# Kernel optimization log

Measured on AMD Instinct MI355X. Metric: run time of the kernel, lower is better.

Reference implementation:

```python
import jax, jax.numpy as jnp
import numpy as np

DIM = 1024
HEADS = 16
HEAD_DIM = DIM // HEADS  # 64
WIN = 256
B, N = 4, 4096


def setup_inputs() -> dict:
    key = jax.random.key(0)
    k1, k2, k3 = jax.random.split(key, 3)
    x = jax.random.normal(k1, (B, N, DIM), dtype=jnp.float32)
    # torch nn.Linear weights: [out_features, in_features]
    Wqkv = jax.random.normal(k2, (3 * DIM, DIM), dtype=jnp.float32) * (DIM ** -0.5)
    Wproj = jax.random.normal(k3, (DIM, DIM), dtype=jnp.float32) * (DIM ** -0.5)
    return {"x": x, "Wqkv": Wqkv, "Wproj": Wproj}


def reference(x, Wqkv, Wproj):
    Bs, Ns, C = x.shape
    H, hd, W = HEADS, HEAD_DIM, WIN
    # qkv projection -> [3, B, H, N, hd]
    qkv = (x @ Wqkv.T).reshape(Bs, Ns, 3, H, hd).transpose(2, 0, 3, 1, 4)
    q, k, v = qkv[0], qkv[1], qkv[2]
    q = q * (hd ** -0.5)
    pad = (W - Ns % W) % W
    if pad:
        pw = ((0, 0), (0, 0), (0, pad), (0, 0))
        q = jnp.pad(q, pw)
        k = jnp.pad(k, pw)
        v = jnp.pad(v, pw)
    Np = Ns + pad
    Df = (Np * hd) // W  # flattened feature dim per window row
    q = q.reshape(Bs * H, W, Df)
    k = k.reshape(Bs * H, W, Df)
    v = v.reshape(Bs * H, W, Df)
    attn = jax.nn.softmax(jnp.einsum('bwd,bxd->bwx', q, k), axis=-1)  # [B*H, W, W]
    out = jnp.einsum('bwx,bxd->bwd', attn, v)
    out = out.reshape(Bs, H, Np, hd)[:, :, :Ns, :].transpose(0, 2, 1, 3).reshape(Bs, Ns, C)
    return out @ Wproj.T
```

## Files before the change

### kernel.cpp

```cpp
#include <hip/hip_runtime.h>
#include <hip/hip_bf16.h>
#include <stdint.h>


using u16 = unsigned short;
typedef __attribute__((ext_vector_type(4))) float f32x4;
typedef __attribute__((ext_vector_type(8))) short s16x8;

#define MFMA_BF16(a, b, c) __builtin_amdgcn_mfma_f32_16x16x32_bf16((a), (b), (c), 0, 0, 0)

__device__ __forceinline__ u16 f2bf(float f) {
  union { float f; uint32_t u; } v; v.f = f;
  uint32_t r = v.u + 0x7fffu + ((v.u >> 16) & 1u);
  return (u16)(r >> 16);
}

__device__ __forceinline__ void gld16(const void* g, void* l) {
  auto gp = (const __attribute__((address_space(1))) void*)(uintptr_t)g;
  auto lp = (__attribute__((address_space(3))) void*)(uint32_t)(uintptr_t)l;
  __builtin_amdgcn_global_load_lds(gp, lp, 16, 0, 0);
}

__global__ __launch_bounds__(256) void cvt3(const float* __restrict__ x,
                                            const float* __restrict__ w1,
                                            const float* __restrict__ w2,
                                            u16* __restrict__ ox,
                                            u16* __restrict__ ow1,
                                            u16* __restrict__ ow2) {
  const int stride = gridDim.x * blockDim.x;
  for (int i = blockIdx.x * blockDim.x + threadIdx.x; i < 2621440; i += stride) {
    const float* src; u16* dst; int j;
    if (i < 2097152)      { src = x;  dst = ox;  j = i; }
    else if (i < 2490368) { src = w1; dst = ow1; j = i - 2097152; }
    else                  { src = w2; dst = ow2; j = i - 2490368; }
    const float4* p = (const float4*)src + (size_t)j * 2;
    float4 a = p[0], b = p[1];
    s16x8 r;
    r[0] = (short)f2bf(a.x); r[1] = (short)f2bf(a.y);
    r[2] = (short)f2bf(a.z); r[3] = (short)f2bf(a.w);
    r[4] = (short)f2bf(b.x); r[5] = (short)f2bf(b.y);
    r[6] = (short)f2bf(b.z); r[7] = (short)f2bf(b.w);
    *(s16x8*)(dst + (size_t)j * 8) = r;
  }
}

template <bool QS, bool F32OUT, int GN>
__global__ __launch_bounds__(512, 2) void gemm256(const u16* __restrict__ A,
                                                  const u16* __restrict__ W,
                                                  void* __restrict__ C) {
  __shared__ alignas(16) u16 lds[2 * 16384];
  const int tid = threadIdx.x;
  const int wv = tid >> 6, lane = tid & 63;
  const int fr = lane & 15, fg = lane >> 4;
  const int wm = wv >> 2, wn = wv & 3;
  const int N = GN * 256;

  const int nwg = 64 * GN;
  const int p = blockIdx.x;
  const int logical = (p & 7) * (nwg >> 3) + (p >> 3);
  const int bm = logical / GN, bn = logical % GN;

  const int srow = tid >> 2;
  const int skg = (tid & 3) ^ ((tid >> 3) & 3);

  const u16* As = A + (size_t)(bm * 256 + srow) * 1024 + skg * 8;
  const u16* Ws = W + (size_t)(bn * 256 + srow) * 1024 + skg * 8;

  const f32x4 fz = {0.f, 0.f, 0.f, 0.f};
  f32x4 acc[8][4];
#pragma unroll
  for (int i = 0; i < 8; ++i)
#pragma unroll
    for (int j = 0; j < 4; ++j) acc[i][j] = fz;

  auto STAGE = [&](int t) {
    u16* dst = lds + (t & 1) * 16384;
    const int k0 = t * 32;
    gld16(As + k0,          dst + wv * 512);
    gld16(As + 131072 + k0, dst + 4096 + wv * 512);
    gld16(Ws + k0,          dst + 8192 + wv * 512);
    gld16(Ws + 131072 + k0, dst + 12288 + wv * 512);
  };

  STAGE(0);
  asm volatile("s_waitcnt vmcnt(0)" ::: "memory");
  __builtin_amdgcn_s_barrier();

  const int rsw = (fg ^ ((fr >> 1) & 3)) * 8;
  const int aoff = (wm * 128 + fr) * 32 + rsw;
  const int boff = 8192 + (wn * 64 + fr) * 32 + rsw;

  for (int t = 0; t < 32; ++t) {
    const u16* buf = lds + (t & 1) * 16384;
    s16x8 a0[4], a1[4], bv[4];

#pragma unroll
    for (int mi = 0; mi < 4; ++mi)
      a0[mi] = *(const s16x8*)(buf + aoff + mi * 512);
#pragma unroll
    for (int ni = 0; ni < 4; ++ni)
      bv[ni] = *(const s16x8*)(buf + boff + ni * 512);
    __builtin_amdgcn_sched_barrier(0);
#pragma unroll
    for (int mi = 0; mi < 4; ++mi)
      a1[mi] = *(const s16x8*)(buf + aoff + (4 + mi) * 512);

    if (t < 31) STAGE(t + 1);

    asm volatile("s_waitcnt lgkmcnt(4)" ::: "memory");
    __builtin_amdgcn_sched_barrier(0);
    __builtin_amdgcn_s_setprio(1);
#pragma unroll
    for (int ni = 0; ni < 4; ++ni)
#pragma unroll
      for (int mi = 0; mi < 4; ++mi)
        acc[mi][ni] = MFMA_BF16(a0[mi], bv[ni], acc[mi][ni]);
    __builtin_amdgcn_s_setprio(0);

    asm volatile("s_waitcnt lgkmcnt(0)" ::: "memory");
    __builtin_amdgcn_sched_barrier(0);
    __builtin_amdgcn_s_setprio(1);
#pragma unroll
    for (int ni = 0; ni < 4; ++ni)
#pragma unroll
      for (int mi = 0; mi < 4; ++mi)
        acc[4 + mi][ni] = MFMA_BF16(a1[mi], bv[ni], acc[4 + mi][ni]);
    __builtin_amdgcn_s_setprio(0);

    if (t < 31) {
      asm volatile("s_waitcnt vmcnt(0)" ::: "memory");
      __builtin_amdgcn_s_barrier();
    }
  }

  const float scale = (QS && bn < 4) ? 0.125f : 1.0f;
#pragma unroll
  for (int mi = 0; mi < 8; ++mi)
#pragma unroll
    for (int ni = 0; ni < 4; ++ni) {
      const int row = bm * 256 + wm * 128 + mi * 16 + fg * 4;
      const int col = bn * 256 + wn * 64 + ni * 16 + fr;
      if (F32OUT) {
        float* cp = (float*)C + (size_t)row * N + col;
#pragma unroll
        for (int r = 0; r < 4; ++r) cp[(size_t)r * N] = acc[mi][ni][r] * scale;
      } else {
        u16* cp = (u16*)C + (size_t)row * N + col;
#pragma unroll
        for (int r = 0; r < 4; ++r) cp[(size_t)r * N] = f2bf(acc[mi][ni][r] * scale);
      }
    }
}

__global__ __launch_bounds__(512) void attn_win(const u16* __restrict__ qkv,
                                                u16* __restrict__ attn) {
  const int bid = blockIdx.x;
  const int bh = (bid & 7) + ((bid >> 5) << 3);
  const int qb = (bid >> 3) & 3;
  const int b = bh >> 4, h = bh & 15;

  const int tid = threadIdx.x;
  const int wv = tid >> 6, lane = tid & 63;
  const int fr = lane & 15, fg = lane >> 4;

  __shared__ alignas(16) char smem[74752];
  u16* lP = (u16*)smem;
  const int SB = 33792;
  float* redm = (float*)(smem + SB);
  float* reds = (float*)(smem + SB + 2048);

  const size_t qbase = (size_t)b * 4096 * 3072;
  const int sg = (lane & 3) ^ ((lane >> 3) & 3);

  const int krow = tid >> 2;
  const u16* Ksrc = qkv + qbase + (size_t)(krow * 16) * 3072 + 1024 + h * 64 + sg * 8;
  const int qrow = (wv & 3) * 16 + (lane >> 2);
  const u16* Qsrc = qkv + qbase + (size_t)((qb * 64 + qrow) * 16) * 3072 + h * 64 + sg * 8;

  auto STAGE_QK = [&](int t) {
    u16* qd = (u16*)(smem + SB + (t & 1) * 4096);
    u16* kd = (u16*)(smem + SB + 8192 + (t & 1) * 16384);
    const int dofs = (t >> 1) * 3072 + (t & 1) * 32;
    gld16(Ksrc + dofs, kd + wv * 512);
    gld16(Ksrc + (size_t)128 * 16 * 3072 + dofs, kd + 4096 + wv * 512);
    if (wv < 4) gld16(Qsrc + dofs, qd + wv * 512);
  };

  const f32x4 fz = {0.f, 0.f, 0.f, 0.f};
  f32x4 acc[4][2];
#pragma unroll
  for (int i = 0; i < 4; ++i)
#pragma unroll
    for (int j = 0; j < 2; ++j) acc[i][j] = fz;

  const int rsw = (fg ^ ((fr >> 1) & 3)) * 8;

  STAGE_QK(0);
  asm volatile("s_waitcnt vmcnt(0)" ::: "memory");
  __builtin_amdgcn_s_barrier();

  for (int kt = 0; kt < 32; ++kt) {
    const u16* qbuf = (const u16*)(smem + SB + (kt & 1) * 4096);
    const u16* kbuf = (const u16*)(smem + SB + 8192 + (kt & 1) * 16384);
    if (kt < 31) STAGE_QK(kt + 1);

    s16x8 qa[4], kb[2];
#pragma unroll
    for (int mi = 0; mi < 4; ++mi)
      qa[mi] = *(const s16x8*)(qbuf + (mi * 16 + fr) * 32 + rsw);
#pragma unroll
    for (int ni = 0; ni < 2; ++ni)
      kb[ni] = *(const s16x8*)(kbuf + (wv * 32 + ni * 16 + fr) * 32 + rsw);

    asm volatile("s_waitcnt lgkmcnt(0)" ::: "memory");
    __builtin_amdgcn_sched_barrier(0);
    __builtin_amdgcn_s_setprio(1);
#pragma unroll
    for (int ni = 0; ni < 2; ++ni)
#pragma unroll
      for (int mi = 0; mi < 4; ++mi)
        acc[mi][ni] = MFMA_BF16(qa[mi], kb[ni], acc[mi][ni]);
    __builtin_amdgcn_s_setprio(0);

    if (kt < 31) {
      asm volatile("s_waitcnt vmcnt(0)" ::: "memory");
      __builtin_amdgcn_s_barrier();
    }
  }
  __syncthreads();

  float rmax[4][4], rnrm[4][4];
#pragma unroll
  for (int mi = 0; mi < 4; ++mi)
#pragma unroll
    for (int r = 0; r < 4; ++r) {
      float m = fmaxf(acc[mi][0][r], acc[mi][1][r]);
      for (int o = 1; o < 16; o <<= 1) m = fmaxf(m, __shfl_xor(m, o));
      rmax[mi][r] = m;
    }
  if (fr == 0) {
#pragma unroll
    for (int mi = 0; mi < 4; ++mi)
#pragma unroll
      for (int r = 0; r < 4; ++r) redm[wv * 64 + mi * 16 + fg * 4 + r] = rmax[mi][r];
  }
  __syncthreads();
#pragma unroll
  for (int mi = 0; mi < 4; ++mi)
#pragma unroll
    for (int r = 0; r < 4; ++r) {
      const int row = mi * 16 + fg * 4 + r;
      float m = redm[row];
#pragma unroll
      for (int w = 1; w < 8; ++w) m = fmaxf(m, redm[w * 64 + row]);
      rmax[mi][r] = m;
    }
#pragma unroll
  for (int mi = 0; mi < 4; ++mi)
#pragma unroll
    for (int r = 0; r < 4; ++r) {
      float s = 0.f;
#pragma unroll
      for (int ni = 0; ni < 2; ++ni) {
        float p = exp2f((acc[mi][ni][r] - rmax[mi][r]) * 1.4426950408889634f);
        acc[mi][ni][r] = p;
        s += p;
      }
      for (int o = 1; o < 16; o <<= 1) s += __shfl_xor(s, o);
      rnrm[mi][r] = s;
    }
  __syncthreads();
  if (fr == 0) {
#pragma unroll
    for (int mi = 0; mi < 4; ++mi)
#pragma unroll
      for (int r = 0; r < 4; ++r) reds[wv * 64 + mi * 16 + fg * 4 + r] = rnrm[mi][r];
  }
  __syncthreads();
#pragma unroll
  for (int mi = 0; mi < 4; ++mi)
#pragma unroll
    for (int r = 0; r < 4; ++r) {
      const int row = mi * 16 + fg * 4 + r;
      float s = reds[row];
#pragma unroll
      for (int w = 1; w < 8; ++w) s += reds[w * 64 + row];
      rnrm[mi][r] = 1.f / s;
    }
#pragma unroll
  for (int mi = 0; mi < 4; ++mi)
#pragma unroll
    for (int ni = 0; ni < 2; ++ni)
#pragma unroll
      for (int r = 0; r < 4; ++r)
        lP[(mi * 16 + fg * 4 + r) * 264 + wv * 32 + ni * 16 + fr] =
            f2bf(acc[mi][ni][r] * rnrm[mi][r]);
  __syncthreads();

  u16* lVt0 = (u16*)(smem + SB);
  u16* lVt1 = (u16*)(smem + SB + 20480);
  const int ld = tid & 255;
  const int jb = tid >> 8;

  for (int nc = 0; nc < 4; ++nc) {
    const int d = nc * 256 + ld;
    const u16* Vcol = qkv + qbase + (size_t)(d >> 6) * 3072 + 2048 + h * 64 + (d & 63);

    f32x4 oacc[4][2];
#pragma unroll
    for (int i = 0; i < 4; ++i)
#pragma unroll
      for (int j = 0; j < 2; ++j) oacc[i][j] = fz;

    u16 va[2][8];
    auto VLOAD = [&](int xt) {
#pragma unroll
      for (int jj = 0; jj < 2; ++jj) {
        const int xo = (jb + 2 * jj) * 8;
        const u16* g = Vcol + (size_t)((xt * 32 + xo) * 16) * 3072;
#pragma unroll
        for (int i = 0; i < 8; ++i) va[jj][i] = g[(size_t)i * 16 * 3072];
      }
    };
    auto VWRITE = [&](u16* buf) {
#pragma unroll
      for (int jj = 0; jj < 2; ++jj) {
        const int xo = (jb + 2 * jj) * 8;
        s16x8 v;
#pragma unroll
        for (int i = 0; i < 8; ++i) v[i] = (short)va[jj][i];
        *(s16x8*)(buf + ld * 40 + xo) = v;
      }
    };

    VLOAD(0);
    VWRITE(lVt0);

#pragma unroll 1
    for (int xt = 0; xt < 8; ++xt) {
      u16* cur = (xt & 1) ? lVt1 : lVt0;
      u16* nxt = (xt & 1) ? lVt0 : lVt1;
      __syncthreads();

      if (xt < 7) VLOAD(xt + 1);

      s16x8 pa[4], vb[2];
#pragma unroll
      for (int mi = 0; mi < 4; ++mi)
        pa[mi] = *(const s16x8*)(lP + (mi * 16 + fr) * 264 + xt * 32 + fg * 8);
#pragma unroll
      for (int ni = 0; ni < 2; ++ni)
        vb[ni] = *(const s16x8*)(cur + (wv * 32 + ni * 16 + fr) * 40 + fg * 8);

      asm volatile("s_waitcnt lgkmcnt(0)" ::: "memory");
      __builtin_amdgcn_sched_barrier(0);
      __builtin_amdgcn_s_setprio(1);
#pragma unroll
      for (int ni = 0; ni < 2; ++ni)
#pragma unroll
        for (int mi = 0; mi < 4; ++mi)
          oacc[mi][ni] = MFMA_BF16(pa[mi], vb[ni], oacc[mi][ni]);
      __builtin_amdgcn_s_setprio(0);

      if (xt < 7) VWRITE(nxt);
    }
    __syncthreads();

#pragma unroll
    for (int mi = 0; mi < 4; ++mi)
#pragma unroll
      for (int ni = 0; ni < 2; ++ni) {
        const int row = mi * 16 + fg * 4;
        const int dd = nc * 256 + wv * 32 + ni * 16 + fr;
        const int pp = dd >> 6, e = dd & 63;
        const size_t base =
            (size_t)(b * 4096 + (qb * 64 + row) * 16 + pp) * 1024 + h * 64 + e;
#pragma unroll
        for (int r = 0; r < 4; ++r)
          attn[base + (size_t)r * 16 * 1024] = f2bf(oacc[mi][ni][r]);
      }
  }
}

extern "C" void kernel_launch(void* const* d_in, const int* in_sizes, int n_in,
                              void* d_out, int out_size, void* d_ws, size_t ws_size,
                              hipStream_t stream) {
  (void)in_sizes; (void)n_in; (void)out_size; (void)ws_size;
  const float* x = (const float*)d_in[0];
  const float* wqkv = (const float*)d_in[1];
  const float* wproj = (const float*)d_in[2];
  float* out = (float*)d_out;

  char* ws = (char*)d_ws;
  u16* qkv = (u16*)ws;
  u16* xbf = (u16*)(ws + 100663296);
  u16* attn = xbf;
  u16* wqkvb = (u16*)(ws + 134217728);
  u16* wprojb = (u16*)(ws + 140509184);

  cvt3<<<2048, 256, 0, stream>>>(x, wqkv, wproj, xbf, wqkvb, wprojb);
  gemm256<true, false, 12><<<768, 512, 0, stream>>>(xbf, wqkvb, qkv);
  attn_win<<<256, 512, 0, stream>>>(qkv, attn);
  gemm256<false, true, 4><<<256, 512, 0, stream>>>(attn, wprojb, out);
}
```

Baseline: 231.0 us.

## Fuse x fp32-to-bf16 conversion into QKV GEMM and retile projection GEMM

After: 276.0 us. 1.19x slower.

```diff
diff --git a/kernel.cpp b/kernel.cpp
--- a/kernel.cpp
+++ b/kernel.cpp
@@ -21,18 +21,15 @@
   __builtin_amdgcn_global_load_lds(gp, lp, 16, 0, 0);
 }
 
-__global__ __launch_bounds__(256) void cvt3(const float* __restrict__ x,
-                                            const float* __restrict__ w1,
+__global__ __launch_bounds__(256) void cvtW(const float* __restrict__ w1,
                                             const float* __restrict__ w2,
-                                            u16* __restrict__ ox,
                                             u16* __restrict__ ow1,
                                             u16* __restrict__ ow2) {
   const int stride = gridDim.x * blockDim.x;
-  for (int i = blockIdx.x * blockDim.x + threadIdx.x; i < 2621440; i += stride) {
+  for (int i = blockIdx.x * blockDim.x + threadIdx.x; i < 524288; i += stride) {
     const float* src; u16* dst; int j;
-    if (i < 2097152)      { src = x;  dst = ox;  j = i; }
-    else if (i < 2490368) { src = w1; dst = ow1; j = i - 2097152; }
-    else                  { src = w2; dst = ow2; j = i - 2490368; }
+    if (i < 393216) { src = w1; dst = ow1; j = i; }
+    else            { src = w2; dst = ow2; j = i - 393216; }
     const float4* p = (const float4*)src + (size_t)j * 2;
     float4 a = p[0], b = p[1];
     s16x8 r;
@@ -44,10 +41,10 @@
   }
 }
 
-template <bool QS, bool F32OUT, int GN>
-__global__ __launch_bounds__(512, 2) void gemm256(const u16* __restrict__ A,
-                                                  const u16* __restrict__ W,
-                                                  void* __restrict__ C) {
+template <int GN>
+__global__ __launch_bounds__(512, 2) void gemm_qkv(const float* __restrict__ X,
+                                                   const u16* __restrict__ W,
+                                                   u16* __restrict__ C) {
   __shared__ alignas(16) u16 lds[2 * 16384];
   const int tid = threadIdx.x;
   const int wv = tid >> 6, lane = tid & 63;
@@ -62,9 +59,12 @@
 
   const int srow = tid >> 2;
   const int skg = (tid & 3) ^ ((tid >> 3) & 3);
-
-  const u16* As = A + (size_t)(bm * 256 + srow) * 1024 + skg * 8;
   const u16* Ws = W + (size_t)(bn * 256 + srow) * 1024 + skg * 8;
+
+  const int arow = tid >> 1;
+  const float* Xs = X + (size_t)(bm * 256 + arow) * 1024 + (tid & 1) * 16;
+  const int ag0 = (tid & 1) * 2;
+  const int asw = (arow >> 1) & 3;
 
   const f32x4 fz = {0.f, 0.f, 0.f, 0.f};
   f32x4 acc[8][4];
@@ -73,13 +73,137 @@
 #pragma unroll
     for (int j = 0; j < 4; ++j) acc[i][j] = fz;
 
+  float4 av0, av1, av2, av3;
+  auto STAGE_B = [&](int t) {
+    u16* dst = lds + (t & 1) * 16384 + 8192;
+    const int k0 = t * 32;
+    gld16(Ws + k0,          dst + wv * 512);
+    gld16(Ws + 131072 + k0, dst + 4096 + wv * 512);
+  };
+  auto LOAD_A = [&](int t) {
+    const float4* s = (const float4*)(Xs + t * 32);
+    av0 = s[0]; av1 = s[1]; av2 = s[2]; av3 = s[3];
+  };
+  auto WRITE_A = [&](int t) {
+    u16* dst = lds + (t & 1) * 16384 + arow * 32;
+    s16x8 v0, v1;
+    v0[0] = (short)f2bf(av0.x); v0[1] = (short)f2bf(av0.y);
+    v0[2] = (short)f2bf(av0.z); v0[3] = (short)f2bf(av0.w);
+    v0[4] = (short)f2bf(av1.x); v0[5] = (short)f2bf(av1.y);
+    v0[6] = (short)f2bf(av1.z); v0[7] = (short)f2bf(av1.w);
+    v1[0] = (short)f2bf(av2.x); v1[1] = (short)f2bf(av2.y);
+    v1[2] = (short)f2bf(av2.z); v1[3] = (short)f2bf(av2.w);
+    v1[4] = (short)f2bf(av3.x); v1[5] = (short)f2bf(av3.y);
+    v1[6] = (short)f2bf(av3.z); v1[7] = (short)f2bf(av3.w);
+    *(s16x8*)(dst + (ag0 ^ asw) * 8) = v0;
+    *(s16x8*)(dst + ((ag0 + 1) ^ asw) * 8) = v1;
+  };
+
+  STAGE_B(0);
+  LOAD_A(0);
+  asm volatile("s_waitcnt vmcnt(0)" ::: "memory");
+  WRITE_A(0);
+  asm volatile("s_waitcnt lgkmcnt(0)" ::: "memory");
+  __builtin_amdgcn_s_barrier();
+
+  const int rsw = (fg ^ ((fr >> 1) & 3)) * 8;
+  const int aoff = (wm * 128 + fr) * 32 + rsw;
+  const int boff = 8192 + (wn * 64 + fr) * 32 + rsw;
+
+  for (int t = 0; t < 32; ++t) {
+    const u16* buf = lds + (t & 1) * 16384;
+    s16x8 a0[4], a1[4], bv[4];
+
+#pragma unroll
+    for (int mi = 0; mi < 4; ++mi)
+      a0[mi] = *(const s16x8*)(buf + aoff + mi * 512);
+#pragma unroll
+    for (int ni = 0; ni < 4; ++ni)
+      bv[ni] = *(const s16x8*)(buf + boff + ni * 512);
+    __builtin_amdgcn_sched_barrier(0);
+#pragma unroll
+    for (int mi = 0; mi < 4; ++mi)
+      a1[mi] = *(const s16x8*)(buf + aoff + (4 + mi) * 512);
+
+    if (t < 31) {
+      STAGE_B(t + 1);
+      LOAD_A(t + 1);
+    }
+
+    asm volatile("s_waitcnt lgkmcnt(4)" ::: "memory");
+    __builtin_amdgcn_sched_barrier(0);
+    __builtin_amdgcn_s_setprio(1);
+#pragma unroll
+    for (int ni = 0; ni < 4; ++ni)
+#pragma unroll
+      for (int mi = 0; mi < 4; ++mi)
+        acc[mi][ni] = MFMA_BF16(a0[mi], bv[ni], acc[mi][ni]);
+    __builtin_amdgcn_s_setprio(0);
+
+    asm volatile("s_waitcnt lgkmcnt(0)" ::: "memory");
+    __builtin_amdgcn_sched_barrier(0);
+    __builtin_amdgcn_s_setprio(1);
+#pragma unroll
+    for (int ni = 0; ni < 4; ++ni)
+#pragma unroll
+      for (int mi = 0; mi < 4; ++mi)
+        acc[4 + mi][ni] = MFMA_BF16(a1[mi], bv[ni], acc[4 + mi][ni]);
+    __builtin_amdgcn_s_setprio(0);
+
+    if (t < 31) {
+      asm volatile("s_waitcnt vmcnt(0)" ::: "memory");
+      WRITE_A(t + 1);
+      asm volatile("s_waitcnt lgkmcnt(0)" ::: "memory");
+      __builtin_amdgcn_s_barrier();
+    }
+  }
+
+  const float scale_q = 0.125f;
+#pragma unroll
+  for (int mi = 0; mi < 8; ++mi)
+#pragma unroll
+    for (int ni = 0; ni < 4; ++ni) {
+      const int row = bm * 256 + wm * 128 + mi * 16 + fg * 4;
+      const int col = bn * 256 + wn * 64 + ni * 16 + fr;
+      const float scale = (bn < 4) ? scale_q : 1.0f;
+      u16* cp = C + (size_t)row * N + col;
+#pragma unroll
+      for (int r = 0; r < 4; ++r) cp[(size_t)r * N] = f2bf(acc[mi][ni][r] * scale);
+    }
+}
+
+__global__ __launch_bounds__(512, 2) void gemm_proj(const u16* __restrict__ A,
+                                                    const u16* __restrict__ W,
+                                                    float* __restrict__ C) {
+  __shared__ alignas(16) u16 lds[2 * 12288];
+  const int tid = threadIdx.x;
+  const int wv = tid >> 6, lane = tid & 63;
+  const int fr = lane & 15, fg = lane >> 4;
+  const int wm = wv >> 2, wn = wv & 3;
+
+  const int p = blockIdx.x;
+  const int logical = (p & 7) * 64 + (p >> 3);
+  const int bm = logical >> 2, bn = logical & 3;
+
+  const int srow = tid >> 2;
+  const int skg = (tid & 3) ^ ((tid >> 3) & 3);
+
+  const u16* As = A + (size_t)(bm * 128 + srow) * 1024 + skg * 8;
+  const u16* Ws = W + (size_t)(bn * 256 + srow) * 1024 + skg * 8;
+
+  const f32x4 fz = {0.f, 0.f, 0.f, 0.f};
+  f32x4 acc[4][4];
+#pragma unroll
+  for (int i = 0; i < 4; ++i)
+#pragma unroll
+    for (int j = 0; j < 4; ++j) acc[i][j] = fz;
+
   auto STAGE = [&](int t) {
-    u16* dst = lds + (t & 1) * 16384;
+    u16* dst = lds + (t & 1) * 12288;
     const int k0 = t * 32;
     gld16(As + k0,          dst + wv * 512);
-    gld16(As + 131072 + k0, dst + 4096 + wv * 512);
-    gld16(Ws + k0,          dst + 8192 + wv * 512);
-    gld16(Ws + 131072 + k0, dst + 12288 + wv * 512);
+    gld16(Ws + k0,          dst + 4096 + wv * 512);
+    gld16(Ws + 131072 + k0, dst + 8192 + wv * 512);
   };
 
   STAGE(0);
@@ -87,35 +211,21 @@
   __builtin_amdgcn_s_barrier();
 
   const int rsw = (fg ^ ((fr >> 1) & 3)) * 8;
-  const int aoff = (wm * 128 + fr) * 32 + rsw;
-  const int boff = 8192 + (wn * 64 + fr) * 32 + rsw;
+  const int aoff = (wm * 64 + fr) * 32 + rsw;
+  const int boff = 4096 + (wn * 64 + fr) * 32 + rsw;
 
   for (int t = 0; t < 32; ++t) {
-    const u16* buf = lds + (t & 1) * 16384;
-    s16x8 a0[4], a1[4], bv[4];
-
-#pragma unroll
-    for (int mi = 0; mi < 4; ++mi)
-      a0[mi] = *(const s16x8*)(buf + aoff + mi * 512);
+    const u16* buf = lds + (t & 1) * 12288;
+    s16x8 af[4], bv[4];
+
+#pragma unroll
+    for (int mi = 0; mi < 4; ++mi)
+      af[mi] = *(const s16x8*)(buf + aoff + mi * 512);
 #pragma unroll
     for (int ni = 0; ni < 4; ++ni)
       bv[ni] = *(const s16x8*)(buf + boff + ni * 512);
-    __builtin_amdgcn_sched_barrier(0);
-#pragma unroll
-    for (int mi = 0; mi < 4; ++mi)
-      a1[mi] = *(const s16x8*)(buf + aoff + (4 + mi) * 512);
 
     if (t < 31) STAGE(t + 1);
-
-    asm volatile("s_waitcnt lgkmcnt(4)" ::: "memory");
-    __builtin_amdgcn_sched_barrier(0);
-    __builtin_amdgcn_s_setprio(1);
-#pragma unroll
-    for (int ni = 0; ni < 4; ++ni)
-#pragma unroll
-      for (int mi = 0; mi < 4; ++mi)
-        acc[mi][ni] = MFMA_BF16(a0[mi], bv[ni], acc[mi][ni]);
-    __builtin_amdgcn_s_setprio(0);
 
     asm volatile("s_waitcnt lgkmcnt(0)" ::: "memory");
     __builtin_amdgcn_sched_barrier(0);
@@ -124,7 +234,7 @@
     for (int ni = 0; ni < 4; ++ni)
 #pragma unroll
       for (int mi = 0; mi < 4; ++mi)
-        acc[4 + mi][ni] = MFMA_BF16(a1[mi], bv[ni], acc[4 + mi][ni]);
+        acc[mi][ni] = MFMA_BF16(af[mi], bv[ni], acc[mi][ni]);
     __builtin_amdgcn_s_setprio(0);
 
     if (t < 31) {
@@ -133,22 +243,15 @@
     }
   }
 
-  const float scale = (QS && bn < 4) ? 0.125f : 1.0f;
-#pragma unroll
-  for (int mi = 0; mi < 8; ++mi)
+#pragma unroll
+  for (int mi = 0; mi < 4; ++mi)
 #pragma unroll
     for (int ni = 0; ni < 4; ++ni) {
-      const int row = bm * 256 + wm * 128 + mi * 16 + fg * 4;
+      const int row = bm * 128 + wm * 64 + mi * 16 + fg * 4;
       const int col = bn * 256 + wn * 64 + ni * 16 + fr;
-      if (F32OUT) {
-        float* cp = (float*)C + (size_t)row * N + col;
-#pragma unroll
-        for (int r = 0; r < 4; ++r) cp[(size_t)r * N] = acc[mi][ni][r] * scale;
-      } else {
-        u16* cp = (u16*)C + (size_t)row * N + col;
-#pragma unroll
-        for (int r = 0; r < 4; ++r) cp[(size_t)r * N] = f2bf(acc[mi][ni][r] * scale);
-      }
+      float* cp = C + (size_t)row * 1024 + col;
+#pragma unroll
+      for (int r = 0; r < 4; ++r) cp[(size_t)r * 1024] = acc[mi][ni][r];
     }
 }
 
@@ -393,13 +496,12 @@
 
   char* ws = (char*)d_ws;
   u16* qkv = (u16*)ws;
-  u16* xbf = (u16*)(ws + 100663296);
-  u16* attn = xbf;
+  u16* attn = (u16*)(ws + 100663296);
   u16* wqkvb = (u16*)(ws + 134217728);
   u16* wprojb = (u16*)(ws + 140509184);
 
-  cvt3<<<2048, 256, 0, stream>>>(x, wqkv, wproj, xbf, wqkvb, wprojb);
-  gemm256<true, false, 12><<<768, 512, 0, stream>>>(xbf, wqkvb, qkv);
+  cvtW<<<512, 256, 0, stream>>>(wqkv, wproj, wqkvb, wprojb);
+  gemm_qkv<12><<<768, 512, 0, stream>>>(x, wqkvb, qkv);
   attn_win<<<256, 512, 0, stream>>>(qkv, attn);
-  gemm256<false, true, 4><<<256, 512, 0, stream>>>(attn, wprojb, out);
-}
+  gemm_proj<<<512, 512, 0, stream>>>(attn, wprojb, out);
+}
```
